# Optimization experiments

Hardware: AMD Instinct MI355X
Metric: run time of the kernel (lower is better)

Reference implementation:

```python
import jax, jax.numpy as jnp
import numpy as np

L, D, V, F4 = 12, 768, 50304, 3072
B, T = 4, 1024


def setup_inputs() -> dict:
    key = jax.random.key(0)
    ks = jax.random.split(key, 12)
    s = 0.02
    return {
        "idx": jax.random.randint(ks[0], (B, T), 0, V),
        "targets": jax.random.randint(ks[1], (B, T), 0, V),
        "wte": jax.random.normal(ks[2], (V, D), jnp.float32) * s,  # tied with lm_head
        "pos_embed": jax.random.normal(ks[3], (L, D), jnp.float32),  # per-block (1,1,D) learned pos embed
        "dyt_alpha": jnp.full((L, 3), 0.5, jnp.float32),  # dyt, dyt2, dyt3 alphas
        "dyt_w": jnp.ones((L, 3, D), jnp.float32),
        "dyt_b": jnp.zeros((L, 3, D), jnp.float32),
        "Wq": jax.random.normal(ks[4], (L, D, D), jnp.float32) * s,
        "Wk": jax.random.normal(ks[5], (L, D, D), jnp.float32) * s,
        "Wv": jax.random.normal(ks[6], (L, D, D), jnp.float32) * s,
        "Wp": jax.random.normal(ks[7], (L, D, D), jnp.float32) * s,
        "bp": jnp.zeros((L, D), jnp.float32),
        "We": jax.random.normal(ks[8], (L, F4, D), jnp.float32) * s,
        "be": jnp.zeros((L, F4), jnp.float32),
        "Wc": jax.random.normal(ks[9], (L, D, F4), jnp.float32) * s,
        "bc": jnp.zeros((L, D), jnp.float32),
    }


def _dyt(x, a, w, b):
    return jnp.tanh(a * x) * w + b


def _forward(idx, targets, wte, pos_embed, dyt_alpha, dyt_w, dyt_b,
             Wq, Wk, Wv, Wp, bp, We, be, Wc, bc):
    b, t = idx.shape
    x = wte[idx]  # (b,t,D)
    pos = jnp.arange(t)
    pbias = -jnp.abs(pos[None, :] - pos[:, None]).astype(x.dtype)  # (t,t) ALiBi-style bias
    scale = 1.0 / np.sqrt(D)  # note: source scales by sqrt(emb_dim), not head dim
    total_kl = jnp.asarray(0.0, x.dtype)
    for l in range(L):
        xl = x + pos_embed[l][None, None, :]
        prior = _dyt(xl, dyt_alpha[l, 2], dyt_w[l, 2], dyt_b[l, 2])  # dyt3
        h = _dyt(xl, dyt_alpha[l, 0], dyt_w[l, 0], dyt_b[l, 0])      # dyt (dropout=0)
        Q = jnp.einsum('btd,od->bto', h, Wq[l])
        K = jnp.einsum('btd,od->bto', h, Wk[l])
        Vv = jnp.einsum('btd,od->bto', h, Wv[l])
        scores = jnp.einsum('btd,bsd->bts', Q, K) * scale + pbias  # (b,t,t), no causal mask
        aw = jax.nn.softmax(scores, axis=-1)
        ao = jnp.einsum('bts,bsd->btd', aw, Vv)
        ao = jnp.einsum('btd,od->bto', ao, Wp[l]) + bp[l]
        h2 = _dyt(ao, dyt_alpha[l, 1], dyt_w[l, 1], dyt_b[l, 1])     # dyt2
        h2 = jax.nn.gelu(jnp.einsum('btd,fd->btf', h2, We[l]) + be[l], approximate=False)
        h2 = jnp.einsum('btf,df->btd', h2, Wc[l]) + bc[l]
        posterior = h2 + prior
        m = 0.5 * (prior + posterior)
        lm = jax.nn.log_softmax(m, axis=-1)
        mp = jnp.exp(lm)
        lp = jax.nn.log_softmax(prior, axis=-1)
        lq = jax.nn.log_softmax(posterior, axis=-1)
        # F.kl_div(log_p, q, reduction='batchmean') = sum(q*(log q - log_p)) / batch
        kl = 0.5 * (jnp.sum(mp * (lm - lp)) + jnp.sum(mp * (lm - lq))) / b
        total_kl = total_kl + kl
        x = posterior
    logits = jnp.einsum('btd,vd->btv', x[:, -1:, :], wte)  # (b,1,V)
    full_logits = jnp.einsum('btd,vd->btv', x, wte)
    lsm = jax.nn.log_softmax(full_logits, axis=-1)
    nll = -jnp.take_along_axis(lsm, targets[..., None], axis=-1).squeeze(-1)
    loss = jnp.mean(nll) + total_kl * 0.1
    return logits, loss


def reference(idx, targets, wte, pos_embed, dyt_alpha, dyt_w, dyt_b,
              Wq, Wk, Wv, Wp, bp, We, be, Wc, bc):
    return _forward(idx, targets, wte, pos_embed, dyt_alpha, dyt_w, dyt_b,
                    Wq, Wk, Wv, Wp, bp, We, be, Wc, bc)
```

## Files before the change

kernel.cpp:

```cpp
#include <hip/hip_runtime.h>
#include <hip/hip_bf16.h>

typedef __attribute__((ext_vector_type(8))) short bf16x8;
typedef __attribute__((ext_vector_type(4))) float f32x4;

__device__ __forceinline__ short f2bf(float f) {
  unsigned u = __float_as_uint(f);
  u = u + 0x7fffu + ((u >> 16) & 1u);
  return (short)(u >> 16);
}
__device__ __forceinline__ float bf2f(short s) {
  return __uint_as_float(((unsigned)(unsigned short)s) << 16);
}

#define GLOB_CAST(p) ((const __attribute__((address_space(1))) void*)(p))
#define LDS_CAST(p) ((__attribute__((address_space(3))) void*)(p))
#define GLL16(g, l) __builtin_amdgcn_global_load_lds(GLOB_CAST(g), LDS_CAST(l), 16, 0, 0)

constexpr int EP_BF16 = 0, EP_SCORES = 1, EP_DYT = 2, EP_GELU = 3, EP_PRIOR = 4;

__global__ __launch_bounds__(256) void cvt_k(const float* __restrict__ src,
                                             short* __restrict__ dst, long n4) {
  const long s = (long)blockIdx.x * 256 + threadIdx.x;
  if (s >= n4) return;
  float4 v = ((const float4*)src)[s];
  short4 o = {f2bf(v.x), f2bf(v.y), f2bf(v.z), f2bf(v.w)};
  ((short4*)dst)[s] = o;
}

__global__ __launch_bounds__(256) void cvt_layer_k(
    const float* __restrict__ wq, const float* __restrict__ wk,
    const float* __restrict__ wv, const float* __restrict__ wp,
    const float* __restrict__ we, const float* __restrict__ wc,
    short* __restrict__ dst) {
  const long s = (long)blockIdx.x * 256 + threadIdx.x;
  const long e = s * 4;
  const float* src; long off;
  if (e < 589824)        { src = wq; off = e; }
  else if (e < 1179648)  { src = wk; off = e - 589824; }
  else if (e < 1769472)  { src = wv; off = e - 1179648; }
  else if (e < 2359296)  { src = wp; off = e - 1769472; }
  else if (e < 4718592)  { src = we; off = e - 2359296; }
  else                   { src = wc; off = e - 4718592; }
  float4 v = *(const float4*)(src + off);
  short4 o = {f2bf(v.x), f2bf(v.y), f2bf(v.z), f2bf(v.w)};
  *(short4*)(dst + e) = o;
}

__global__ __launch_bounds__(256) void embed_head_k(
    const int* __restrict__ idx, const float* __restrict__ wte,
    const float* __restrict__ pos, const float* __restrict__ alp,
    const float* __restrict__ w, const float* __restrict__ b,
    float* __restrict__ x, float* __restrict__ prior, short* __restrict__ h) {
  const long s = (long)blockIdx.x * 256 + threadIdx.x;
  const long row = s / 192;
  const int c4 = (int)(s % 192);
  float4 xv = ((const float4*)(wte + (long)idx[row] * 768))[c4];
  ((float4*)x)[s] = xv;
  float4 pv = ((const float4*)pos)[c4];
  float4 w0 = ((const float4*)w)[c4];
  float4 b0 = ((const float4*)b)[c4];
  float4 w2 = ((const float4*)(w + 1536))[c4];
  float4 b2 = ((const float4*)(b + 1536))[c4];
  const float a0 = alp[0], a2 = alp[2];
  float4 xl = {xv.x + pv.x, xv.y + pv.y, xv.z + pv.z, xv.w + pv.w};
  float4 pr = {tanhf(a2 * xl.x) * w2.x + b2.x, tanhf(a2 * xl.y) * w2.y + b2.y,
               tanhf(a2 * xl.z) * w2.z + b2.z, tanhf(a2 * xl.w) * w2.w + b2.w};
  ((float4*)prior)[s] = pr;
  short4 hh = {f2bf(tanhf(a0 * xl.x) * w0.x + b0.x),
               f2bf(tanhf(a0 * xl.y) * w0.y + b0.y),
               f2bf(tanhf(a0 * xl.z) * w0.z + b0.z),
               f2bf(tanhf(a0 * xl.w) * w0.w + b0.w)};
  ((short4*)h)[s] = hh;
}

template <int EP, int TN>
__global__ __launch_bounds__(256, 2) void gemm_bt(
    const short* __restrict__ A, const short* __restrict__ B,
    void* __restrict__ Cv, int K, int lda, int ldb, int ldc,
    long sA, long sB, long sC,
    const float* __restrict__ bias, const float* __restrict__ dw,
    const float* __restrict__ db, const float* __restrict__ alp,
    const float* __restrict__ prior, float scale) {
  constexpr int NF = TN / 32;
  __shared__ short As[128 * 64];
  __shared__ short Bs[TN * 64];
  const int tid = threadIdx.x, lane = tid & 63;
  const int wr = tid >> 7, wc = (tid >> 6) & 1;
  const long rowBase = (long)blockIdx.y * 128;
  const long colBase = (long)blockIdx.x * TN;
  const short* Ab = A + (long)blockIdx.z * sA;
  const short* Bb = B + (long)blockIdx.z * sB;
  const int srow = tid >> 3, sseg = tid & 7;
  const int ssegS = sseg ^ (srow & 7);

  f32x4 acc[4][NF];
#pragma unroll
  for (int m = 0; m < 4; ++m)
#pragma unroll
    for (int n = 0; n < NF; ++n) acc[m][n] = (f32x4){0.f, 0.f, 0.f, 0.f};

  const int q = lane >> 4, cl = lane & 15;
  const int rsw = cl & 7;

  for (int kt = 0; kt < K; kt += 64) {
#pragma unroll
    for (int i = 0; i < 4; ++i)
      GLL16(Ab + (rowBase + i * 32 + srow) * (long)lda + kt + ssegS * 8,
            As + ((i * 32 + srow) * 64 + sseg * 8));
#pragma unroll
    for (int i = 0; i < TN / 32; ++i)
      GLL16(Bb + (colBase + i * 32 + srow) * (long)ldb + kt + ssegS * 8,
            Bs + ((i * 32 + srow) * 64 + sseg * 8));
    __syncthreads();
#pragma unroll
    for (int kk = 0; kk < 2; ++kk) {
      const int sw = ((kk * 4 + q) ^ rsw) << 3;
      bf16x8 af[4], bfr[NF];
#pragma unroll
      for (int m = 0; m < 4; ++m)
        af[m] = *(const bf16x8*)&As[(wr * 64 + m * 16 + cl) * 64 + sw];
#pragma unroll
      for (int n = 0; n < NF; ++n)
        bfr[n] = *(const bf16x8*)&Bs[(wc * (TN / 2) + n * 16 + cl) * 64 + sw];
#pragma unroll
      for (int m = 0; m < 4; ++m)
#pragma unroll
        for (int n = 0; n < NF; ++n)
          acc[m][n] = __builtin_amdgcn_mfma_f32_16x16x32_bf16(af[m], bfr[n], acc[m][n], 0, 0, 0);
    }
    __syncthreads();
  }

#pragma unroll
  for (int m = 0; m < 4; ++m) {
#pragma unroll
    for (int n = 0; n < NF; ++n) {
#pragma unroll
      for (int j = 0; j < 4; ++j) {
        long r = rowBase + wr * 64 + m * 16 + q * 4 + j;
        long c = colBase + wc * (TN / 2) + n * 16 + cl;
        float v = acc[m][n][j];
        if constexpr (EP == EP_SCORES) {
          ((short*)Cv)[(long)blockIdx.z * sC + r * ldc + c] = f2bf(v * scale);
        } else if constexpr (EP == EP_BF16) {
          ((short*)Cv)[(long)blockIdx.z * sC + r * ldc + c] = f2bf(v);
        } else if constexpr (EP == EP_DYT) {
          float xv = v + bias[c];
          ((short*)Cv)[r * (long)ldc + c] = f2bf(tanhf(alp[0] * xv) * dw[c] + db[c]);
        } else if constexpr (EP == EP_GELU) {
          float xv = v + bias[c];
          ((short*)Cv)[r * (long)ldc + c] = f2bf(0.5f * xv * (1.f + erff(xv * 0.70710678118654752f)));
        } else if constexpr (EP == EP_PRIOR) {
          ((float*)Cv)[r * (long)ldc + c] = v + bias[c] + prior[r * (long)ldc + c];
        }
      }
    }
  }
}

__global__ __launch_bounds__(256) void transp_k(const short* __restrict__ V,
                                                short* __restrict__ Vt, int ldv) {
  __shared__ short t[32][33];
  const int b = blockIdx.z;
  const int d0 = blockIdx.x * 32, t0 = blockIdx.y * 32;
  const int tx = threadIdx.x & 31, ty = threadIdx.x >> 5;
  const short* Vb = V + (long)b * 1024 * ldv;
  short* Tb = Vt + (long)b * 768 * 1024;
#pragma unroll
  for (int i = 0; i < 4; ++i)
    t[ty + i * 8][tx] = Vb[(long)(t0 + ty + i * 8) * ldv + d0 + tx];
  __syncthreads();
#pragma unroll
  for (int i = 0; i < 4; ++i)
    Tb[(long)(d0 + ty + i * 8) * 1024 + t0 + tx] = t[tx][ty + i * 8];
}

__global__ __launch_bounds__(256) void softmax_k(short* __restrict__ sc) {
  const int lane = threadIdx.x & 63;
  const long row = (long)blockIdx.x * 4 + (threadIdx.x >> 6);
  const int t = (int)(row & 1023);
  short* p = sc + row * 1024;
  const int c0 = lane * 16;
  bf16x8 a = *(const bf16x8*)(p + c0);
  bf16x8 b = *(const bf16x8*)(p + c0 + 8);
  float v[16];
  float mx = -3e38f;
#pragma unroll
  for (int i = 0; i < 8; ++i) {
    v[i] = bf2f(a[i]) - fabsf((float)(t - (c0 + i)));
    v[i + 8] = bf2f(b[i]) - fabsf((float)(t - (c0 + 8 + i)));
  }
#pragma unroll
  for (int i = 0; i < 16; ++i) mx = fmaxf(mx, v[i]);
#pragma unroll
  for (int o = 1; o < 64; o <<= 1) mx = fmaxf(mx, __shfl_xor(mx, o));
  float e[16];
  float s = 0.f;
#pragma unroll
  for (int i = 0; i < 16; ++i) { e[i] = __expf(v[i] - mx); s += e[i]; }
#pragma unroll
  for (int o = 1; o < 64; o <<= 1) s += __shfl_xor(s, o);
  const float inv = 1.f / s;
  bf16x8 o0, o1;
#pragma unroll
  for (int i = 0; i < 8; ++i) {
    o0[i] = f2bf(e[i] * inv);
    o1[i] = f2bf(e[i + 8] * inv);
  }
  *(bf16x8*)(p + c0) = o0;
  *(bf16x8*)(p + c0 + 8) = o1;
}

__global__ __launch_bounds__(256) void tail_k(
    float* __restrict__ prior, const float* __restrict__ post,
    const float* __restrict__ pos_n, const float* __restrict__ alp_n,
    const float* __restrict__ w_n, const float* __restrict__ b_n,
    short* __restrict__ h, short* __restrict__ xbf,
    double* __restrict__ acc, int last) {
  const int lane = threadIdx.x & 63;
  const long row = (long)blockIdx.x * 4 + (threadIdx.x >> 6);
  float* pp = prior + row * 768;
  const float* qq = post + row * 768;
  float p[12], q[12];
#pragma unroll
  for (int i = 0; i < 12; ++i) { p[i] = pp[lane + i * 64]; q[i] = qq[lane + i * 64]; }
  float mp = -3e38f, mq = -3e38f, mm = -3e38f;
#pragma unroll
  for (int i = 0; i < 12; ++i) {
    float m = 0.5f * (p[i] + q[i]);
    mp = fmaxf(mp, p[i]); mq = fmaxf(mq, q[i]); mm = fmaxf(mm, m);
  }
#pragma unroll
  for (int o = 1; o < 64; o <<= 1) {
    mp = fmaxf(mp, __shfl_xor(mp, o));
    mq = fmaxf(mq, __shfl_xor(mq, o));
    mm = fmaxf(mm, __shfl_xor(mm, o));
  }
  float sp = 0.f, sq = 0.f, sm = 0.f;
#pragma unroll
  for (int i = 0; i < 12; ++i) {
    sp += __expf(p[i] - mp);
    sq += __expf(q[i] - mq);
    sm += __expf(0.5f * (p[i] + q[i]) - mm);
  }
#pragma unroll
  for (int o = 1; o < 64; o <<= 1) {
    sp += __shfl_xor(sp, o); sq += __shfl_xor(sq, o); sm += __shfl_xor(sm, o);
  }
  const float lseP = mp + logf(sp), lseQ = mq + logf(sq), lseM = mm + logf(sm);
  float kl = 0.f;
#pragma unroll
  for (int i = 0; i < 12; ++i) {
    float m = 0.5f * (p[i] + q[i]);
    float lm = m - lseM;
    kl += __expf(lm) * (2.f * lm - (p[i] - lseP) - (q[i] - lseQ));
  }
#pragma unroll
  for (int o = 1; o < 64; o <<= 1) kl += __shfl_xor(kl, o);
  if (lane == 0) atomicAdd(&acc[0], (double)kl);

  if (last) {
#pragma unroll
    for (int i = 0; i < 12; ++i) xbf[row * 768 + lane + i * 64] = f2bf(q[i]);
  } else {
    const float a0 = alp_n[0], a2 = alp_n[2];
#pragma unroll
    for (int i = 0; i < 12; ++i) {
      const int col = lane + i * 64;
      float xl = q[i] + pos_n[col];
      pp[col] = tanhf(a2 * xl) * w_n[1536 + col] + b_n[1536 + col];
      h[row * 768 + col] = f2bf(tanhf(a0 * xl) * w_n[col] + b_n[col]);
    }
  }
}

__global__ __launch_bounds__(256, 2) void lse_gemm_k(
    const short* __restrict__ Xb, const short* __restrict__ Wt,
    float* __restrict__ pm, float* __restrict__ ps,
    float* __restrict__ logits_out, int G) {
  __shared__ short As[128 * 64];
  __shared__ short Bs[128 * 64];
  __shared__ float pmx[2][128], psm[2][128], rm[128], rs[128];
  const int tid = threadIdx.x, lane = tid & 63;
  const int wr = tid >> 7, wc = (tid >> 6) & 1;
  const int g = blockIdx.x;
  const long rowBase = (long)blockIdx.y * 128;
  const int srow = tid >> 3, sseg = tid & 7;
  const int ssegS = sseg ^ (srow & 7);
  const int q = lane >> 4, cl = lane & 15;
  const int rsw = cl & 7;
  if (tid < 128) { rm[tid] = -3e38f; rs[tid] = 0.f; }

  for (int tile = g; tile < 393; tile += G) {
    const long colBase = (long)tile * 128;
    f32x4 acc[4][4];
#pragma unroll
    for (int m = 0; m < 4; ++m)
#pragma unroll
      for (int n = 0; n < 4; ++n) acc[m][n] = (f32x4){0.f, 0.f, 0.f, 0.f};

    for (int kt = 0; kt < 768; kt += 64) {
#pragma unroll
      for (int i = 0; i < 4; ++i) {
        GLL16(Xb + (rowBase + i * 32 + srow) * 768L + kt + ssegS * 8,
              As + ((i * 32 + srow) * 64 + sseg * 8));
        GLL16(Wt + (colBase + i * 32 + srow) * 768L + kt + ssegS * 8,
              Bs + ((i * 32 + srow) * 64 + sseg * 8));
      }
      __syncthreads();
#pragma unroll
      for (int kk = 0; kk < 2; ++kk) {
        const int sw = ((kk * 4 + q) ^ rsw) << 3;
        bf16x8 af[4], bfr[4];
#pragma unroll
        for (int m = 0; m < 4; ++m)
          af[m] = *(const bf16x8*)&As[(wr * 64 + m * 16 + cl) * 64 + sw];
#pragma unroll
        for (int n = 0; n < 4; ++n)
          bfr[n] = *(const bf16x8*)&Bs[(wc * 64 + n * 16 + cl) * 64 + sw];
#pragma unroll
        for (int m = 0; m < 4; ++m)
#pragma unroll
          for (int n = 0; n < 4; ++n)
            acc[m][n] = __builtin_amdgcn_mfma_f32_16x16x32_bf16(af[m], bfr[n], acc[m][n], 0, 0, 0);
      }
      __syncthreads();
    }

#pragma unroll
    for (int m = 0; m < 4; ++m)
#pragma unroll
      for (int n = 0; n < 4; ++n)
#pragma unroll
        for (int j = 0; j < 4; ++j) {
          long r = rowBase + wr * 64 + m * 16 + q * 4 + j;
          if ((r & 1023) == 1023) {
            long c = colBase + wc * 64 + n * 16 + cl;
            logits_out[(r >> 10) * 50304 + c] = acc[m][n][j];
          }
        }

#pragma unroll
    for (int m = 0; m < 4; ++m) {
#pragma unroll
      for (int j = 0; j < 4; ++j) {
        float mx = acc[m][0][j];
#pragma unroll
        for (int n = 1; n < 4; ++n) mx = fmaxf(mx, acc[m][n][j]);
#pragma unroll
        for (int o = 1; o < 16; o <<= 1) mx = fmaxf(mx, __shfl_xor(mx, o));
        float sm = 0.f;
#pragma unroll
        for (int n = 0; n < 4; ++n) sm += __expf(acc[m][n][j] - mx);
#pragma unroll
        for (int o = 1; o < 16; o <<= 1) sm += __shfl_xor(sm, o);
        if (cl == 0) {
          int lr = wr * 64 + m * 16 + q * 4 + j;
          pmx[wc][lr] = mx;
          psm[wc][lr] = sm;
        }
      }
    }
    __syncthreads();
    if (tid < 128) {
      float m0 = pmx[0][tid], m1 = pmx[1][tid];
      float m2 = fmaxf(m0, m1);
      float s2 = psm[0][tid] * __expf(m0 - m2) + psm[1][tid] * __expf(m1 - m2);
      float mo = rm[tid], mn = fmaxf(mo, m2);
      rs[tid] = rs[tid] * __expf(mo - mn) + s2 * __expf(m2 - mn);
      rm[tid] = mn;
    }
    __syncthreads();
  }
  if (tid < 128) {
    long row = rowBase + tid;
    pm[row * G + g] = rm[tid];
    ps[row * G + g] = rs[tid];
  }
}

__global__ __launch_bounds__(256) void tlog_k(const short* __restrict__ xbf,
                                              const short* __restrict__ wtebf,
                                              const int* __restrict__ targets,
                                              float* __restrict__ tlog) {
  const int lane = threadIdx.x & 63;
  const long row = (long)blockIdx.x * 4 + (threadIdx.x >> 6);
  const long tgt = targets[row];
  const short* a = xbf + row * 768;
  const short* b = wtebf + tgt * 768;
  float s = 0.f;
#pragma unroll
  for (int i = 0; i < 12; ++i) s += bf2f(a[lane + i * 64]) * bf2f(b[lane + i * 64]);
#pragma unroll
  for (int o = 1; o < 64; o <<= 1) s += __shfl_xor(s, o);
  if (lane == 0) tlog[row] = s;
}

__global__ __launch_bounds__(256) void stage2_k(const float* __restrict__ pm,
                                                const float* __restrict__ ps,
                                                const float* __restrict__ tlog,
                                                double* __restrict__ acc, int G) {
  const long row = (long)blockIdx.x * 256 + threadIdx.x;
  float M = -3e38f;
  for (int gi = 0; gi < G; ++gi) M = fmaxf(M, pm[row * G + gi]);
  float S = 0.f;
  for (int gi = 0; gi < G; ++gi) S += ps[row * G + gi] * __expf(pm[row * G + gi] - M);
  float nll = (M + logf(S)) - tlog[row];
#pragma unroll
  for (int o = 1; o < 64; o <<= 1) nll += __shfl_xor(nll, o);
  if ((threadIdx.x & 63) == 0) atomicAdd(&acc[1], (double)nll);
}

__global__ void finalize_k(const double* __restrict__ acc, float* __restrict__ out) {
  if (threadIdx.x == 0)
    out[201216] = (float)(acc[1] / 4096.0 + 0.1 * 0.5 * acc[0] / 4.0);
}

constexpr size_t OFF_WTEBF = 0;
constexpr size_t OFF_LW    = 77266944;
constexpr size_t OFF_X     = 91422720;
constexpr size_t OFF_PRIOR = 104005632;
constexpr size_t OFF_HB    = 116588544;
constexpr size_t OFF_U1    = 122880000;
constexpr size_t OFF_QKV   = OFF_U1;
constexpr size_t OFF_VT    = OFF_U1 + 18874368;
constexpr size_t OFF_E     = OFF_U1;
constexpr size_t OFF_SC    = 148045824;
constexpr size_t OFF_AO    = 164823040;
constexpr size_t OFF_XBF   = 171114496;
constexpr size_t OFF_PM    = 177405952;
constexpr size_t OFF_PS    = 177799168;
constexpr size_t OFF_TLOG  = 178192384;
constexpr size_t OFF_ACC   = 178208768;
constexpr size_t WS_NEED   = 178208784;

extern "C" void kernel_launch(void* const* d_in, const int* in_sizes, int n_in,
                              void* d_out, int out_size, void* d_ws, size_t ws_size,
                              hipStream_t stream) {
  const int* idx = (const int*)d_in[0];
  const int* targets = (const int*)d_in[1];
  const float* wte = (const float*)d_in[2];
  const float* pos = (const float*)d_in[3];
  const float* dalpha = (const float*)d_in[4];
  const float* dytw = (const float*)d_in[5];
  const float* dytb = (const float*)d_in[6];
  const float* Wq = (const float*)d_in[7];
  const float* Wk = (const float*)d_in[8];
  const float* Wv = (const float*)d_in[9];
  const float* Wp = (const float*)d_in[10];
  const float* bp = (const float*)d_in[11];
  const float* We = (const float*)d_in[12];
  const float* be = (const float*)d_in[13];
  const float* Wc = (const float*)d_in[14];
  const float* bc = (const float*)d_in[15];
  float* out = (float*)d_out;

  if (ws_size < WS_NEED) return;
  char* ws = (char*)d_ws;
  short* WTEBF = (short*)(ws + OFF_WTEBF);
  short* LW = (short*)(ws + OFF_LW);
  float* X = (float*)(ws + OFF_X);
  float* PRIOR = (float*)(ws + OFF_PRIOR);
  short* HB = (short*)(ws + OFF_HB);
  short* QKVB = (short*)(ws + OFF_QKV);
  short* VT = (short*)(ws + OFF_VT);
  short* E = (short*)(ws + OFF_E);
  short* SC = (short*)(ws + OFF_SC);
  short* AO = (short*)(ws + OFF_AO);
  short* XBF = (short*)(ws + OFF_XBF);
  float* PM = (float*)(ws + OFF_PM);
  float* PS = (float*)(ws + OFF_PS);
  float* TLOG = (float*)(ws + OFF_TLOG);
  double* ACC = (double*)(ws + OFF_ACC);

  hipMemsetAsync(ACC, 0, 16, stream);
  cvt_k<<<37728, 256, 0, stream>>>(wte, WTEBF, 9658368);
  embed_head_k<<<3072, 256, 0, stream>>>(idx, wte, pos, dalpha, dytw, dytb, X, PRIOR, HB);

  const float scale = 0.03608439182435161f;

  for (int l = 0; l < 12; ++l) {
    cvt_layer_k<<<6912, 256, 0, stream>>>(Wq + (long)l * 589824, Wk + (long)l * 589824,
                                          Wv + (long)l * 589824, Wp + (long)l * 589824,
                                          We + (long)l * 2359296, Wc + (long)l * 2359296, LW);
    gemm_bt<EP_BF16, 128><<<dim3(18, 32, 1), 256, 0, stream>>>(
        HB, LW, QKVB, 768, 768, 768, 2304, 0, 0, 0,
        nullptr, nullptr, nullptr, nullptr, nullptr, 0.f);
    transp_k<<<dim3(24, 32, 4), 256, 0, stream>>>(QKVB + 1536, VT, 2304);
    gemm_bt<EP_SCORES, 64><<<dim3(16, 8, 4), 256, 0, stream>>>(
        QKVB, QKVB + 768, SC, 768, 2304, 2304, 1024,
        2359296, 2359296, 1048576, nullptr, nullptr, nullptr, nullptr, nullptr, scale);
    softmax_k<<<1024, 256, 0, stream>>>(SC);
    gemm_bt<EP_BF16, 64><<<dim3(12, 8, 4), 256, 0, stream>>>(
        SC, VT, AO, 1024, 1024, 1024, 768, 1048576, 786432, 786432,
        nullptr, nullptr, nullptr, nullptr, nullptr, 0.f);
    gemm_bt<EP_DYT, 64><<<dim3(12, 32, 1), 256, 0, stream>>>(
        AO, LW + 1769472, HB, 768, 768, 768, 768, 0, 0, 0,
        bp + l * 768, dytw + l * 2304 + 768, dytb + l * 2304 + 768,
        dalpha + l * 3 + 1, nullptr, 0.f);
    gemm_bt<EP_GELU, 128><<<dim3(24, 32, 1), 256, 0, stream>>>(
        HB, LW + 2359296, E, 768, 768, 768, 3072, 0, 0, 0,
        be + l * 3072, nullptr, nullptr, nullptr, nullptr, 0.f);
    gemm_bt<EP_PRIOR, 64><<<dim3(12, 32, 1), 256, 0, stream>>>(
        E, LW + 4718592, X, 3072, 3072, 3072, 768, 0, 0, 0,
        bc + l * 768, nullptr, nullptr, nullptr, PRIOR, 0.f);
    tail_k<<<1024, 256, 0, stream>>>(PRIOR, X, pos + (l + 1) * 768,
                                     dalpha + (l + 1) * 3, dytw + (l + 1) * 2304,
                                     dytb + (l + 1) * 2304, HB, XBF, ACC, l == 11);
  }

  lse_gemm_k<<<dim3(24, 32), 256, 0, stream>>>(XBF, WTEBF, PM, PS, out, 24);
  tlog_k<<<1024, 256, 0, stream>>>(XBF, WTEBF, targets, TLOG);
  stage2_k<<<16, 256, 0, stream>>>(PM, PS, TLOG, ACC, 24);
  finalize_k<<<1, 64, 0, stream>>>(ACC, out);
}
```

Before: 3.089 ms.

## Fuse softmax with V transpose and prefetch next-layer weight conversion into tail

Merges the V transpose into the softmax launch as extra blocks and moves it after the scores GEMM. The per-layer weight bf16 conversion is folded into the tail kernel as extra blocks that convert the next layer's weights into a double-buffered LW region. Layer 0's conversion is hoisted before the loop. This cuts launch count and lets the conversion run alongside the tail work, at the cost of a larger workspace and more blocks in the tail grid.

```diff
diff --git a/kernel.cpp b/kernel.cpp
--- a/kernel.cpp
+++ b/kernel.cpp
@@ -159,65 +159,88 @@
   }
 }
 
-__global__ __launch_bounds__(256) void transp_k(const short* __restrict__ V,
-                                                short* __restrict__ Vt, int ldv) {
-  __shared__ short t[32][33];
-  const int b = blockIdx.z;
-  const int d0 = blockIdx.x * 32, t0 = blockIdx.y * 32;
-  const int tx = threadIdx.x & 31, ty = threadIdx.x >> 5;
-  const short* Vb = V + (long)b * 1024 * ldv;
-  short* Tb = Vt + (long)b * 768 * 1024;
-#pragma unroll
-  for (int i = 0; i < 4; ++i)
-    t[ty + i * 8][tx] = Vb[(long)(t0 + ty + i * 8) * ldv + d0 + tx];
-  __syncthreads();
-#pragma unroll
-  for (int i = 0; i < 4; ++i)
-    Tb[(long)(d0 + ty + i * 8) * 1024 + t0 + tx] = t[tx][ty + i * 8];
-}
-
-__global__ __launch_bounds__(256) void softmax_k(short* __restrict__ sc) {
-  const int lane = threadIdx.x & 63;
-  const long row = (long)blockIdx.x * 4 + (threadIdx.x >> 6);
-  const int t = (int)(row & 1023);
-  short* p = sc + row * 1024;
-  const int c0 = lane * 16;
-  bf16x8 a = *(const bf16x8*)(p + c0);
-  bf16x8 b = *(const bf16x8*)(p + c0 + 8);
-  float v[16];
-  float mx = -3e38f;
-#pragma unroll
-  for (int i = 0; i < 8; ++i) {
-    v[i] = bf2f(a[i]) - fabsf((float)(t - (c0 + i)));
-    v[i + 8] = bf2f(b[i]) - fabsf((float)(t - (c0 + 8 + i)));
-  }
-#pragma unroll
-  for (int i = 0; i < 16; ++i) mx = fmaxf(mx, v[i]);
-#pragma unroll
-  for (int o = 1; o < 64; o <<= 1) mx = fmaxf(mx, __shfl_xor(mx, o));
-  float e[16];
-  float s = 0.f;
-#pragma unroll
-  for (int i = 0; i < 16; ++i) { e[i] = __expf(v[i] - mx); s += e[i]; }
-#pragma unroll
-  for (int o = 1; o < 64; o <<= 1) s += __shfl_xor(s, o);
-  const float inv = 1.f / s;
-  bf16x8 o0, o1;
-#pragma unroll
-  for (int i = 0; i < 8; ++i) {
-    o0[i] = f2bf(e[i] * inv);
-    o1[i] = f2bf(e[i + 8] * inv);
-  }
-  *(bf16x8*)(p + c0) = o0;
-  *(bf16x8*)(p + c0 + 8) = o1;
-}
-
-__global__ __launch_bounds__(256) void tail_k(
+__global__ __launch_bounds__(256) void softmax_transp_k(
+    short* __restrict__ sc, const short* __restrict__ qkvb,
+    short* __restrict__ vt) {
+  if (blockIdx.x < 1024) {
+    const int lane = threadIdx.x & 63;
+    const long row = (long)blockIdx.x * 4 + (threadIdx.x >> 6);
+    const int t = (int)(row & 1023);
+    short* p = sc + row * 1024;
+    const int c0 = lane * 16;
+    bf16x8 a = *(const bf16x8*)(p + c0);
+    bf16x8 b = *(const bf16x8*)(p + c0 + 8);
+    float v[16];
+    float mx = -3e38f;
+#pragma unroll
+    for (int i = 0; i < 8; ++i) {
+      v[i] = bf2f(a[i]) - fabsf((float)(t - (c0 + i)));
+      v[i + 8] = bf2f(b[i]) - fabsf((float)(t - (c0 + 8 + i)));
+    }
+#pragma unroll
+    for (int i = 0; i < 16; ++i) mx = fmaxf(mx, v[i]);
+#pragma unroll
+    for (int o = 1; o < 64; o <<= 1) mx = fmaxf(mx, __shfl_xor(mx, o));
+    float e[16];
+    float s = 0.f;
+#pragma unroll
+    for (int i = 0; i < 16; ++i) { e[i] = __expf(v[i] - mx); s += e[i]; }
+#pragma unroll
+    for (int o = 1; o < 64; o <<= 1) s += __shfl_xor(s, o);
+    const float inv = 1.f / s;
+    bf16x8 o0, o1;
+#pragma unroll
+    for (int i = 0; i < 8; ++i) {
+      o0[i] = f2bf(e[i] * inv);
+      o1[i] = f2bf(e[i + 8] * inv);
+    }
+    *(bf16x8*)(p + c0) = o0;
+    *(bf16x8*)(p + c0 + 8) = o1;
+  } else {
+    __shared__ short tbuf[32][33];
+    const int t = blockIdx.x - 1024;
+    const int b = t & 3;
+    const int rest = t >> 2;
+    const int d0 = (rest % 24) * 32, t0 = (rest / 24) * 32;
+    const int tx = threadIdx.x & 31, ty = threadIdx.x >> 5;
+    const short* Vb = qkvb + (long)b * 1024 * 2304 + 1536;
+    short* Tb = vt + (long)b * 768 * 1024;
+#pragma unroll
+    for (int i = 0; i < 4; ++i)
+      tbuf[ty + i * 8][tx] = Vb[(long)(t0 + ty + i * 8) * 2304 + d0 + tx];
+    __syncthreads();
+#pragma unroll
+    for (int i = 0; i < 4; ++i)
+      Tb[(long)(d0 + ty + i * 8) * 1024 + t0 + tx] = tbuf[tx][ty + i * 8];
+  }
+}
+
+__global__ __launch_bounds__(256) void tail_cvt_k(
     float* __restrict__ prior, const float* __restrict__ post,
     const float* __restrict__ pos_n, const float* __restrict__ alp_n,
     const float* __restrict__ w_n, const float* __restrict__ b_n,
     short* __restrict__ h, short* __restrict__ xbf,
-    double* __restrict__ acc, int last) {
+    double* __restrict__ acc, int last,
+    const float* __restrict__ wq, const float* __restrict__ wk,
+    const float* __restrict__ wv, const float* __restrict__ wp,
+    const float* __restrict__ we, const float* __restrict__ wc,
+    short* __restrict__ lwdst) {
+  if (blockIdx.x >= 1024) {
+    if (last) return;
+    const long s = (long)(blockIdx.x - 1024) * 256 + threadIdx.x;
+    const long e = s * 4;
+    const float* src; long off;
+    if (e < 589824)        { src = wq; off = e; }
+    else if (e < 1179648)  { src = wk; off = e - 589824; }
+    else if (e < 1769472)  { src = wv; off = e - 1179648; }
+    else if (e < 2359296)  { src = wp; off = e - 1769472; }
+    else if (e < 4718592)  { src = we; off = e - 2359296; }
+    else                   { src = wc; off = e - 4718592; }
+    float4 v = *(const float4*)(src + off);
+    short4 o = {f2bf(v.x), f2bf(v.y), f2bf(v.z), f2bf(v.w)};
+    *(short4*)(lwdst + e) = o;
+    return;
+  }
   const int lane = threadIdx.x & 63;
   const long row = (long)blockIdx.x * 4 + (threadIdx.x >> 6);
   float* pp = prior + row * 768;
@@ -419,21 +442,21 @@
 
 constexpr size_t OFF_WTEBF = 0;
 constexpr size_t OFF_LW    = 77266944;
-constexpr size_t OFF_X     = 91422720;
-constexpr size_t OFF_PRIOR = 104005632;
-constexpr size_t OFF_HB    = 116588544;
-constexpr size_t OFF_U1    = 122880000;
+constexpr size_t OFF_X     = 105578496;
+constexpr size_t OFF_PRIOR = 118161408;
+constexpr size_t OFF_HB    = 130744320;
+constexpr size_t OFF_U1    = 137035776;
 constexpr size_t OFF_QKV   = OFF_U1;
 constexpr size_t OFF_VT    = OFF_U1 + 18874368;
 constexpr size_t OFF_E     = OFF_U1;
-constexpr size_t OFF_SC    = 148045824;
-constexpr size_t OFF_AO    = 164823040;
-constexpr size_t OFF_XBF   = 171114496;
-constexpr size_t OFF_PM    = 177405952;
-constexpr size_t OFF_PS    = 177799168;
-constexpr size_t OFF_TLOG  = 178192384;
-constexpr size_t OFF_ACC   = 178208768;
-constexpr size_t WS_NEED   = 178208784;
+constexpr size_t OFF_SC    = 162201600;
+constexpr size_t OFF_AO    = 170590208;
+constexpr size_t OFF_XBF   = 176881664;
+constexpr size_t OFF_PM    = 183173120;
+constexpr size_t OFF_PS    = 183566336;
+constexpr size_t OFF_TLOG  = 183959552;
+constexpr size_t OFF_ACC   = 183975936;
+constexpr size_t WS_NEED   = 183975952;
 
 extern "C" void kernel_launch(void* const* d_in, const int* in_sizes, int n_in,
                               void* d_out, int out_size, void* d_ws, size_t ws_size,
@@ -476,38 +499,40 @@
 
   hipMemsetAsync(ACC, 0, 16, stream);
   cvt_k<<<37728, 256, 0, stream>>>(wte, WTEBF, 9658368);
+  cvt_layer_k<<<6912, 256, 0, stream>>>(Wq, Wk, Wv, Wp, We, Wc, LW);
   embed_head_k<<<3072, 256, 0, stream>>>(idx, wte, pos, dalpha, dytw, dytb, X, PRIOR, HB);
 
   const float scale = 0.03608439182435161f;
 
   for (int l = 0; l < 12; ++l) {
-    cvt_layer_k<<<6912, 256, 0, stream>>>(Wq + (long)l * 589824, Wk + (long)l * 589824,
-                                          Wv + (long)l * 589824, Wp + (long)l * 589824,
-                                          We + (long)l * 2359296, Wc + (long)l * 2359296, LW);
+    const short* lw = LW + (long)(l & 1) * 7077888;
     gemm_bt<EP_BF16, 128><<<dim3(18, 32, 1), 256, 0, stream>>>(
-        HB, LW, QKVB, 768, 768, 768, 2304, 0, 0, 0,
+        HB, lw, QKVB, 768, 768, 768, 2304, 0, 0, 0,
         nullptr, nullptr, nullptr, nullptr, nullptr, 0.f);
-    transp_k<<<dim3(24, 32, 4), 256, 0, stream>>>(QKVB + 1536, VT, 2304);
     gemm_bt<EP_SCORES, 64><<<dim3(16, 8, 4), 256, 0, stream>>>(
         QKVB, QKVB + 768, SC, 768, 2304, 2304, 1024,
         2359296, 2359296, 1048576, nullptr, nullptr, nullptr, nullptr, nullptr, scale);
-    softmax_k<<<1024, 256, 0, stream>>>(SC);
+    softmax_transp_k<<<4096, 256, 0, stream>>>(SC, QKVB, VT);
     gemm_bt<EP_BF16, 64><<<dim3(12, 8, 4), 256, 0, stream>>>(
         SC, VT, AO, 1024, 1024, 1024, 768, 1048576, 786432, 786432,
         nullptr, nullptr, nullptr, nullptr, nullptr, 0.f);
     gemm_bt<EP_DYT, 64><<<dim3(12, 32, 1), 256, 0, stream>>>(
-        AO, LW + 1769472, HB, 768, 768, 768, 768, 0, 0, 0,
+        AO, lw + 1769472, HB, 768, 768, 768, 768, 0, 0, 0,
         bp + l * 768, dytw + l * 2304 + 768, dytb + l * 2304 + 768,
         dalpha + l * 3 + 1, nullptr, 0.f);
     gemm_bt<EP_GELU, 128><<<dim3(24, 32, 1), 256, 0, stream>>>(
-        HB, LW + 2359296, E, 768, 768, 768, 3072, 0, 0, 0,
+        HB, lw + 2359296, E, 768, 768, 768, 3072, 0, 0, 0,
         be + l * 3072, nullptr, nullptr, nullptr, nullptr, 0.f);
     gemm_bt<EP_PRIOR, 64><<<dim3(12, 32, 1), 256, 0, stream>>>(
-        E, LW + 4718592, X, 3072, 3072, 3072, 768, 0, 0, 0,
+        E, lw + 4718592, X, 3072, 3072, 3072, 768, 0, 0, 0,
         bc + l * 768, nullptr, nullptr, nullptr, PRIOR, 0.f);
-    tail_k<<<1024, 256, 0, stream>>>(PRIOR, X, pos + (l + 1) * 768,
-                                     dalpha + (l + 1) * 3, dytw + (l + 1) * 2304,
-                                     dytb + (l + 1) * 2304, HB, XBF, ACC, l == 11);
+    tail_cvt_k<<<7936, 256, 0, stream>>>(
+        PRIOR, X, pos + (l + 1) * 768, dalpha + (l + 1) * 3,
+        dytw + (l + 1) * 2304, dytb + (l + 1) * 2304, HB, XBF, ACC, l == 11,
+        Wq + (long)(l + 1) * 589824, Wk + (long)(l + 1) * 589824,
+        Wv + (long)(l + 1) * 589824, Wp + (long)(l + 1) * 589824,
+        We + (long)(l + 1) * 2359296, Wc + (long)(l + 1) * 2359296,
+        (short*)(ws + OFF_LW) + (long)((l + 1) & 1) * 7077888);
   }
 
   lse_gemm_k<<<dim3(24, 32), 256, 0, stream>>>(XBF, WTEBF, PM, PS, out, 24);
```

New measurement: 2.974 ms. 1.04x faster.
